# Kernel tuning notes

Hardware: AMD Instinct MI355X
Metric: run time of the kernel (lower is better)

The kernel has to match this reference:

```python
import jax, jax.numpy as jnp
import numpy as np

PZ = 8            # pz half-patch in get_dist_base
P = 2 * PZ        # patch side = 16
C, T, HF, WF = 128, 3, 256, 256
N = 2048          # number of keypoint pairs


def setup_inputs() -> dict:
    key = jax.random.key(0)
    ks = jax.random.split(key, 9)
    response = jax.random.normal(ks[0], (C, T, HF, WF), dtype=jnp.float32)
    ys1 = jax.random.randint(ks[1], (N,), 0, HF - P, dtype=jnp.int32)
    xs1 = jax.random.randint(ks[2], (N,), 0, WF - P, dtype=jnp.int32)
    ts1 = jax.random.randint(ks[3], (N,), 0, T, dtype=jnp.int32)
    ys2 = jax.random.randint(ks[4], (N,), 0, HF - P, dtype=jnp.int32)
    xs2 = jax.random.randint(ks[5], (N,), 0, WF - P, dtype=jnp.int32)
    ts2 = jax.random.randint(ks[6], (N,), 0, T, dtype=jnp.int32)
    pair_type = jax.random.randint(ks[7], (N,), 0, 3, dtype=jnp.int32)  # 0=BG,1=I,2=IS
    powers = 1.0 + jax.random.uniform(ks[8], (3,), dtype=jnp.float32)   # per-type exponent in [1,2)
    plus = jnp.ones((1,), dtype=jnp.float32)
    return dict(response=response, ys1=ys1, xs1=xs1, ts1=ts1,
                ys2=ys2, xs2=xs2, ts2=ts2, pair_type=pair_type,
                powers=powers, plus=plus)


def _gather_patches(response, ts, ys, xs):
    # response: [C, T, Hf, Wf] -> patches [N, C, P, P]
    c = response.shape[0]
    def one(t, y, x):
        return jax.lax.dynamic_slice(response, (0, t, y, x), (c, 1, P, P))[:, 0]
    return jax.vmap(one)(ts, ys, xs)


def _minmax_norm(p):
    # normalize_tensor: min-max over whole patch; identity if max==min
    mn = p.min(axis=(1, 2, 3), keepdims=True)
    mx = p.max(axis=(1, 2, 3), keepdims=True)
    rng = mx - mn
    return jnp.where(rng != 0, (p - mn) / jnp.where(rng == 0, 1.0, rng), p)


def reference(response, ys1, xs1, ts1, ys2, xs2, ts2, pair_type, powers, plus):
    P1 = _minmax_norm(_gather_patches(response, ts1, ys1, xs1))
    P2 = _minmax_norm(_gather_patches(response, ts2, ys2, xs2))
    pw = powers[pair_type][:, None, None, None]            # per-pair exponent
    d = jnp.mean(jnp.abs(P1 - P2) ** pw, axis=(1, 2, 3))   # losscal core, [N]
    per = jnp.where(pair_type == 2, d, 1.0 / (1.0 + d))    # IS -> losscal_1, BG/I -> losscal_2
    per = per + jnp.where(pair_type == 0, 0.0, plus[0] * 0.5)  # + plus/2 for I and IS
    return jnp.mean(per)                                   # lossbase / act
```

## Files before the change

### kernel.cpp

```cpp
#include <hip/hip_runtime.h>
#include <math.h>

#define CC 128
#define TT 3
#define HFD 256
#define WFD 256
#define PP 16
#define NPAIR 2048
#define HW (HFD * WFD)
#define POS (TT * HW)
#define CH_STRIDE POS
#define PATCH_ELEMS (CC * PP * PP)
#define BLOCK 256
#define TP 128

typedef float floatx2 __attribute__((ext_vector_type(2)));
typedef float floatx4 __attribute__((ext_vector_type(4)));

__global__ __launch_bounds__(BLOCK) void transpose_minmax_kernel(
    const float* __restrict__ resp,
    unsigned int* __restrict__ rt32,
    float* __restrict__ cmn, float* __restrict__ cmx) {
    __shared__ unsigned int tile32[TP][33];
    __shared__ float smn[8][TP], smx[8][TP];

    int p0 = blockIdx.x * TP;
    int pc = threadIdx.x & 31;
    int ph = threadIdx.x >> 5;

    const float* bp = resp + p0 + 4 * pc;

    float mn0 = INFINITY, mn1 = INFINITY, mn2 = INFINITY, mn3 = INFINITY;
    float mx0 = -INFINITY, mx1 = -INFINITY, mx2 = -INFINITY, mx3 = -INFINITY;

    #pragma unroll
    for (int k = 0; k < 4; ++k) {
        int q = k * 8 + ph;
        floatx4 l0 = *(const floatx4*)(bp + (size_t)(4 * q + 0) * CH_STRIDE);
        floatx4 l1 = *(const floatx4*)(bp + (size_t)(4 * q + 1) * CH_STRIDE);
        floatx4 l2 = *(const floatx4*)(bp + (size_t)(4 * q + 2) * CH_STRIDE);
        floatx4 l3 = *(const floatx4*)(bp + (size_t)(4 * q + 3) * CH_STRIDE);
        #pragma unroll
        for (int j = 0; j < 4; ++j) {
            float v0 = l0[j], v1 = l1[j], v2 = l2[j], v3 = l3[j];
            float mnj = fminf(fminf(v0, v1), fminf(v2, v3));
            float mxj = fmaxf(fmaxf(v0, v1), fmaxf(v2, v3));
            if (j == 0) { mn0 = fminf(mn0, mnj); mx0 = fmaxf(mx0, mxj); }
            if (j == 1) { mn1 = fminf(mn1, mnj); mx1 = fmaxf(mx1, mxj); }
            if (j == 2) { mn2 = fminf(mn2, mnj); mx2 = fmaxf(mx2, mxj); }
            if (j == 3) { mn3 = fminf(mn3, mnj); mx3 = fmaxf(mx3, mxj); }
            int w = __builtin_amdgcn_cvt_pk_fp8_f32(v0, v1, 0, false);
            w = __builtin_amdgcn_cvt_pk_fp8_f32(v2, v3, w, true);
            tile32[4 * pc + j][q] = (unsigned int)w;
        }
    }
    smn[ph][4 * pc + 0] = mn0; smx[ph][4 * pc + 0] = mx0;
    smn[ph][4 * pc + 1] = mn1; smx[ph][4 * pc + 1] = mx1;
    smn[ph][4 * pc + 2] = mn2; smx[ph][4 * pc + 2] = mx2;
    smn[ph][4 * pc + 3] = mn3; smx[ph][4 * pc + 3] = mx3;
    __syncthreads();

    if (threadIdx.x < TP) {
        int tp = threadIdx.x;
        float mn = smn[0][tp], mx = smx[0][tp];
        #pragma unroll
        for (int h = 1; h < 8; ++h) {
            mn = fminf(mn, smn[h][tp]);
            mx = fmaxf(mx, smx[h][tp]);
        }
        cmn[p0 + tp] = mn;
        cmx[p0 + tp] = mx;
    }

    #pragma unroll
    for (int j = 0; j < 16; ++j) {
        int u   = j * BLOCK + threadIdx.x;
        int pos = u >> 5;
        int c4  = u & 31;
        rt32[(((size_t)(p0 + pos)) << 5) + c4] = tile32[pos][c4];
    }
}

__device__ inline float pw_term(float va, float vb, float sc1, float nsc2, float K, float pw) {
    float d = fmaf(va, sc1, fmaf(vb, nsc2, K));
    return __builtin_amdgcn_exp2f(pw * __builtin_amdgcn_logf(fabsf(d)));
}

__device__ inline float quad_acc(unsigned int wa, unsigned int wb,
                                 float sc1, float nsc2, float K, float pw) {
    floatx2 a0 = __builtin_amdgcn_cvt_pk_f32_fp8((int)wa, false);
    floatx2 a1 = __builtin_amdgcn_cvt_pk_f32_fp8((int)wa, true);
    floatx2 b0 = __builtin_amdgcn_cvt_pk_f32_fp8((int)wb, false);
    floatx2 b1 = __builtin_amdgcn_cvt_pk_f32_fp8((int)wb, true);
    return pw_term(a0.x, b0.x, sc1, nsc2, K, pw) + pw_term(a0.y, b0.y, sc1, nsc2, K, pw)
         + pw_term(a1.x, b1.x, sc1, nsc2, K, pw) + pw_term(a1.y, b1.y, sc1, nsc2, K, pw);
}

__global__ __launch_bounds__(BLOCK) void pair_loss_kernel(
    const uint4* __restrict__ rt,
    const int* __restrict__ ts1, const int* __restrict__ ys1, const int* __restrict__ xs1,
    const int* __restrict__ ts2, const int* __restrict__ ys2, const int* __restrict__ xs2,
    const int* __restrict__ pair_type,
    const float* __restrict__ powers,
    const float* __restrict__ plus,
    const float* __restrict__ cmn, const float* __restrict__ cmx,
    float* __restrict__ per_out) {
    int i = blockIdx.x;
    int t1 = ts1[i], y1 = ys1[i], x1 = xs1[i];
    int t2 = ts2[i], y2 = ys2[i], x2 = xs2[i];
    int p1 = t1 * HW + y1 * WFD + x1;
    int p2 = t2 * HW + y2 * WFD + x2;

    int dy = threadIdx.x >> 4, dx = threadIdx.x & 15;
    int q1 = p1 + dy * WFD + dx;
    int q2 = p2 + dy * WFD + dx;
    float a0 = cmn[q1], a1 = cmx[q1];
    float b0 = cmn[q2], b1 = cmx[q2];
    #pragma unroll
    for (int off = 32; off > 0; off >>= 1) {
        a0 = fminf(a0, __shfl_down(a0, off));
        a1 = fmaxf(a1, __shfl_down(a1, off));
        b0 = fminf(b0, __shfl_down(b0, off));
        b1 = fmaxf(b1, __shfl_down(b1, off));
    }
    __shared__ float red[4][4];
    int wave = threadIdx.x >> 6;
    if ((threadIdx.x & 63) == 0) {
        red[wave][0] = a0; red[wave][1] = a1; red[wave][2] = b0; red[wave][3] = b1;
    }
    __syncthreads();
    float mn1 = fminf(fminf(red[0][0], red[1][0]), fminf(red[2][0], red[3][0]));
    float mx1 = fmaxf(fmaxf(red[0][1], red[1][1]), fmaxf(red[2][1], red[3][1]));
    float mn2 = fminf(fminf(red[0][2], red[1][2]), fminf(red[2][2], red[3][2]));
    float mx2 = fmaxf(fmaxf(red[0][3], red[1][3]), fmaxf(red[2][3], red[3][3]));

    float rg1 = mx1 - mn1, rg2 = mx2 - mn2;
    float sc1 = (rg1 != 0.0f) ? (1.0f / rg1) : 1.0f;
    float sh1 = (rg1 != 0.0f) ? mn1 : 0.0f;
    float sc2 = (rg2 != 0.0f) ? (1.0f / rg2) : 1.0f;
    float sh2 = (rg2 != 0.0f) ? mn2 : 0.0f;
    float nsc2 = -sc2;
    float K = sh2 * sc2 - sh1 * sc1;

    int   ptype = pair_type[i];
    float pw    = powers[ptype];

    int c16 = threadIdx.x & 7;
    int pdx = (threadIdx.x >> 3) & 15;
    int dyb = threadIdx.x >> 7;
    const uint4* A = rt + (((size_t)(p1 + pdx)) << 3) + c16;
    const uint4* B = rt + (((size_t)(p2 + pdx)) << 3) + c16;
    const size_t RSTR = (size_t)WFD << 3;

    float acc0 = 0.0f, acc1 = 0.0f;
    #pragma unroll
    for (int j = 0; j < 8; j += 2) {
        size_t offA = (size_t)(dyb + 2 * j) * RSTR;
        size_t offB = (size_t)(dyb + 2 * (j + 1)) * RSTR;
        uint4 wa0 = A[offA];
        uint4 wb0 = B[offA];
        uint4 wa1 = A[offB];
        uint4 wb1 = B[offB];
        acc0 += quad_acc(wa0.x, wb0.x, sc1, nsc2, K, pw);
        acc0 += quad_acc(wa0.y, wb0.y, sc1, nsc2, K, pw);
        acc0 += quad_acc(wa0.z, wb0.z, sc1, nsc2, K, pw);
        acc0 += quad_acc(wa0.w, wb0.w, sc1, nsc2, K, pw);
        acc1 += quad_acc(wa1.x, wb1.x, sc1, nsc2, K, pw);
        acc1 += quad_acc(wa1.y, wb1.y, sc1, nsc2, K, pw);
        acc1 += quad_acc(wa1.z, wb1.z, sc1, nsc2, K, pw);
        acc1 += quad_acc(wa1.w, wb1.w, sc1, nsc2, K, pw);
    }
    float acc = acc0 + acc1;
    for (int off = 32; off > 0; off >>= 1) acc += __shfl_down(acc, off);
    __shared__ float ssum[BLOCK / 64];
    if ((threadIdx.x & 63) == 0) ssum[wave] = acc;
    __syncthreads();
    if (threadIdx.x == 0) {
        float total = ssum[0] + ssum[1] + ssum[2] + ssum[3];
        float dmean = total * (1.0f / (float)PATCH_ELEMS);
        float per = (ptype == 2) ? dmean : (1.0f / (1.0f + dmean));
        per += (ptype == 0) ? 0.0f : plus[0] * 0.5f;
        per_out[i] = per;
    }
}

__global__ __launch_bounds__(BLOCK) void final_mean_kernel(
    const float* __restrict__ per_out, float* __restrict__ out) {
    float acc = 0.0f;
    for (int i = threadIdx.x; i < NPAIR; i += BLOCK) acc += per_out[i];
    for (int off = 32; off > 0; off >>= 1) acc += __shfl_down(acc, off);
    __shared__ float ssum[BLOCK / 64];
    int wave = threadIdx.x >> 6;
    if ((threadIdx.x & 63) == 0) ssum[wave] = acc;
    __syncthreads();
    if (threadIdx.x == 0) {
        float total = ssum[0] + ssum[1] + ssum[2] + ssum[3];
        out[0] = total * (1.0f / (float)NPAIR);
    }
}

extern "C" void kernel_launch(void* const* d_in, const int* in_sizes, int n_in,
                              void* d_out, int out_size, void* d_ws, size_t ws_size,
                              hipStream_t stream) {
    const float* resp      = (const float*)d_in[0];
    const int*   ys1       = (const int*)d_in[1];
    const int*   xs1       = (const int*)d_in[2];
    const int*   ts1       = (const int*)d_in[3];
    const int*   ys2       = (const int*)d_in[4];
    const int*   xs2       = (const int*)d_in[5];
    const int*   ts2       = (const int*)d_in[6];
    const int*   pair_type = (const int*)d_in[7];
    const float* powers    = (const float*)d_in[8];
    const float* plus      = (const float*)d_in[9];
    float*       out       = (float*)d_out;

    unsigned int* rt32 = (unsigned int*)d_ws;
    float* cmn     = (float*)(rt32 + (size_t)POS * 32);
    float* cmx     = cmn + POS;
    float* per_out = cmx + POS;

    transpose_minmax_kernel<<<POS / TP, BLOCK, 0, stream>>>(resp, rt32, cmn, cmx);

    pair_loss_kernel<<<NPAIR, BLOCK, 0, stream>>>(
        (const uint4*)rt32, ts1, ys1, xs1, ts2, ys2, xs2, pair_type, powers, plus,
        cmn, cmx, per_out);

    final_mean_kernel<<<1, BLOCK, 0, stream>>>(per_out, out);
}
```

Measured before the change: 193.0 us.

## Split per-pair normalization constants into separate kernel, move finalization to reduce

Moves the per-pair min/max reduction and normalization-constant computation out of the main pair loss kernel into a new kernel that handles four pairs per block, one wavefront per pair. The main kernel then reads one float4 of constants and no longer needs the shared-memory reduction and barrier before the heavy loop. The per-pair loss transform moves into the final mean kernel. This adds an extra kernel launch and a workspace round trip in exchange for a shorter critical path inside the main kernel.

```diff
diff --git a/kernel.cpp b/kernel.cpp
--- a/kernel.cpp
+++ b/kernel.cpp
@@ -81,6 +81,52 @@
     }
 }
 
+__global__ __launch_bounds__(BLOCK) void pair_const_kernel(
+    const int* __restrict__ ts1, const int* __restrict__ ys1, const int* __restrict__ xs1,
+    const int* __restrict__ ts2, const int* __restrict__ ys2, const int* __restrict__ xs2,
+    const int* __restrict__ pair_type,
+    const float* __restrict__ powers,
+    const float* __restrict__ cmn, const float* __restrict__ cmx,
+    float4* __restrict__ pconst) {
+    int i    = blockIdx.x * 4 + (threadIdx.x >> 6);
+    int lane = threadIdx.x & 63;
+    int p1 = ts1[i] * HW + ys1[i] * WFD + xs1[i];
+    int p2 = ts2[i] * HW + ys2[i] * WFD + xs2[i];
+
+    float a0 = INFINITY, a1 = -INFINITY, b0 = INFINITY, b1 = -INFINITY;
+    #pragma unroll
+    for (int k = 0; k < 4; ++k) {
+        int pos = lane + 64 * k;
+        int dy = pos >> 4, dx = pos & 15;
+        int q1 = p1 + dy * WFD + dx;
+        int q2 = p2 + dy * WFD + dx;
+        a0 = fminf(a0, cmn[q1]);
+        a1 = fmaxf(a1, cmx[q1]);
+        b0 = fminf(b0, cmn[q2]);
+        b1 = fmaxf(b1, cmx[q2]);
+    }
+    #pragma unroll
+    for (int off = 32; off > 0; off >>= 1) {
+        a0 = fminf(a0, __shfl_down(a0, off));
+        a1 = fmaxf(a1, __shfl_down(a1, off));
+        b0 = fminf(b0, __shfl_down(b0, off));
+        b1 = fmaxf(b1, __shfl_down(b1, off));
+    }
+    if (lane == 0) {
+        float rg1 = a1 - a0, rg2 = b1 - b0;
+        float sc1 = (rg1 != 0.0f) ? (1.0f / rg1) : 1.0f;
+        float sh1 = (rg1 != 0.0f) ? a0 : 0.0f;
+        float sc2 = (rg2 != 0.0f) ? (1.0f / rg2) : 1.0f;
+        float sh2 = (rg2 != 0.0f) ? b0 : 0.0f;
+        float4 pc;
+        pc.x = sc1;
+        pc.y = -sc2;
+        pc.z = sh2 * sc2 - sh1 * sc1;
+        pc.w = powers[pair_type[i]];
+        pconst[i] = pc;
+    }
+}
+
 __device__ inline float pw_term(float va, float vb, float sc1, float nsc2, float K, float pw) {
     float d = fmaf(va, sc1, fmaf(vb, nsc2, K));
     return __builtin_amdgcn_exp2f(pw * __builtin_amdgcn_logf(fabsf(d)));
@@ -100,50 +146,14 @@
     const uint4* __restrict__ rt,
     const int* __restrict__ ts1, const int* __restrict__ ys1, const int* __restrict__ xs1,
     const int* __restrict__ ts2, const int* __restrict__ ys2, const int* __restrict__ xs2,
-    const int* __restrict__ pair_type,
-    const float* __restrict__ powers,
-    const float* __restrict__ plus,
-    const float* __restrict__ cmn, const float* __restrict__ cmx,
-    float* __restrict__ per_out) {
+    const float4* __restrict__ pconst,
+    float* __restrict__ part) {
     int i = blockIdx.x;
-    int t1 = ts1[i], y1 = ys1[i], x1 = xs1[i];
-    int t2 = ts2[i], y2 = ys2[i], x2 = xs2[i];
-    int p1 = t1 * HW + y1 * WFD + x1;
-    int p2 = t2 * HW + y2 * WFD + x2;
-
-    int dy = threadIdx.x >> 4, dx = threadIdx.x & 15;
-    int q1 = p1 + dy * WFD + dx;
-    int q2 = p2 + dy * WFD + dx;
-    float a0 = cmn[q1], a1 = cmx[q1];
-    float b0 = cmn[q2], b1 = cmx[q2];
-    #pragma unroll
-    for (int off = 32; off > 0; off >>= 1) {
-        a0 = fminf(a0, __shfl_down(a0, off));
-        a1 = fmaxf(a1, __shfl_down(a1, off));
-        b0 = fminf(b0, __shfl_down(b0, off));
-        b1 = fmaxf(b1, __shfl_down(b1, off));
-    }
-    __shared__ float red[4][4];
-    int wave = threadIdx.x >> 6;
-    if ((threadIdx.x & 63) == 0) {
-        red[wave][0] = a0; red[wave][1] = a1; red[wave][2] = b0; red[wave][3] = b1;
-    }
-    __syncthreads();
-    float mn1 = fminf(fminf(red[0][0], red[1][0]), fminf(red[2][0], red[3][0]));
-    float mx1 = fmaxf(fmaxf(red[0][1], red[1][1]), fmaxf(red[2][1], red[3][1]));
-    float mn2 = fminf(fminf(red[0][2], red[1][2]), fminf(red[2][2], red[3][2]));
-    float mx2 = fmaxf(fmaxf(red[0][3], red[1][3]), fmaxf(red[2][3], red[3][3]));
-
-    float rg1 = mx1 - mn1, rg2 = mx2 - mn2;
-    float sc1 = (rg1 != 0.0f) ? (1.0f / rg1) : 1.0f;
-    float sh1 = (rg1 != 0.0f) ? mn1 : 0.0f;
-    float sc2 = (rg2 != 0.0f) ? (1.0f / rg2) : 1.0f;
-    float sh2 = (rg2 != 0.0f) ? mn2 : 0.0f;
-    float nsc2 = -sc2;
-    float K = sh2 * sc2 - sh1 * sc1;
-
-    int   ptype = pair_type[i];
-    float pw    = powers[ptype];
+    int p1 = ts1[i] * HW + ys1[i] * WFD + xs1[i];
+    int p2 = ts2[i] * HW + ys2[i] * WFD + xs2[i];
+
+    float4 pc = pconst[i];
+    float sc1 = pc.x, nsc2 = pc.y, K = pc.z, pw = pc.w;
 
     int c16 = threadIdx.x & 7;
     int pdx = (threadIdx.x >> 3) & 15;
@@ -173,21 +183,26 @@
     float acc = acc0 + acc1;
     for (int off = 32; off > 0; off >>= 1) acc += __shfl_down(acc, off);
     __shared__ float ssum[BLOCK / 64];
+    int wave = threadIdx.x >> 6;
     if ((threadIdx.x & 63) == 0) ssum[wave] = acc;
     __syncthreads();
     if (threadIdx.x == 0) {
-        float total = ssum[0] + ssum[1] + ssum[2] + ssum[3];
-        float dmean = total * (1.0f / (float)PATCH_ELEMS);
+        part[i] = ssum[0] + ssum[1] + ssum[2] + ssum[3];
+    }
+}
+
+__global__ __launch_bounds__(BLOCK) void final_mean_kernel(
+    const float* __restrict__ part, const int* __restrict__ pair_type,
+    const float* __restrict__ plus, float* __restrict__ out) {
+    float acc = 0.0f;
+    float pl = plus[0] * 0.5f;
+    for (int i = threadIdx.x; i < NPAIR; i += BLOCK) {
+        float dmean = part[i] * (1.0f / (float)PATCH_ELEMS);
+        int ptype = pair_type[i];
         float per = (ptype == 2) ? dmean : (1.0f / (1.0f + dmean));
-        per += (ptype == 0) ? 0.0f : plus[0] * 0.5f;
-        per_out[i] = per;
-    }
-}
-
-__global__ __launch_bounds__(BLOCK) void final_mean_kernel(
-    const float* __restrict__ per_out, float* __restrict__ out) {
-    float acc = 0.0f;
-    for (int i = threadIdx.x; i < NPAIR; i += BLOCK) acc += per_out[i];
+        per += (ptype == 0) ? 0.0f : pl;
+        acc += per;
+    }
     for (int off = 32; off > 0; off >>= 1) acc += __shfl_down(acc, off);
     __shared__ float ssum[BLOCK / 64];
     int wave = threadIdx.x >> 6;
@@ -215,15 +230,18 @@
     float*       out       = (float*)d_out;
 
     unsigned int* rt32 = (unsigned int*)d_ws;
-    float* cmn     = (float*)(rt32 + (size_t)POS * 32);
-    float* cmx     = cmn + POS;
-    float* per_out = cmx + POS;
+    float*  cmn    = (float*)(rt32 + (size_t)POS * 32);
+    float*  cmx    = cmn + POS;
+    float4* pconst = (float4*)(cmx + POS);
+    float*  part   = (float*)(pconst + NPAIR);
 
     transpose_minmax_kernel<<<POS / TP, BLOCK, 0, stream>>>(resp, rt32, cmn, cmx);
 
+    pair_const_kernel<<<NPAIR / 4, BLOCK, 0, stream>>>(
+        ts1, ys1, xs1, ts2, ys2, xs2, pair_type, powers, cmn, cmx, pconst);
+
     pair_loss_kernel<<<NPAIR, BLOCK, 0, stream>>>(
-        (const uint4*)rt32, ts1, ys1, xs1, ts2, ys2, xs2, pair_type, powers, plus,
-        cmn, cmx, per_out);
-
-    final_mean_kernel<<<1, BLOCK, 0, stream>>>(per_out, out);
-}
+        (const uint4*)rt32, ts1, ys1, xs1, ts2, ys2, xs2, pconst, part);
+
+    final_mean_kernel<<<1, BLOCK, 0, stream>>>(part, pair_type, plus, out);
+}
```

Result: slower. 199.7 us (+3.5%).
